# Performance work log

Hardware: AMD Instinct MI355X
Metric: run time of the kernel (lower is better)

## Reference

```python
import jax, jax.numpy as jnp
import numpy as np

B, T, D, H = 4096, 1024, 3, 64


def setup_inputs() -> dict:
    key = jax.random.key(0)
    ks = jax.random.split(key, 10)
    s_ih = 1.0 / np.sqrt(H)
    return {
        "x1": jax.random.normal(ks[0], (B, T, D), dtype=jnp.float32),
        "x2": jax.random.normal(ks[1], (B, T, D), dtype=jnp.float32),
        # PyTorch nn.GRU params, gate order (r, z, n)
        "W_ih": jax.random.uniform(ks[2], (3 * H, D), jnp.float32, -s_ih, s_ih),
        "W_hh": jax.random.uniform(ks[3], (3 * H, H), jnp.float32, -s_ih, s_ih),
        "b_ih": jax.random.uniform(ks[4], (3 * H,), jnp.float32, -s_ih, s_ih),
        "b_hh": jax.random.uniform(ks[5], (3 * H,), jnp.float32, -s_ih, s_ih),
        # MLP head: Linear(64,32) -> ReLU -> Linear(32,1) -> Sigmoid
        "W1": jax.random.uniform(ks[6], (32, H), jnp.float32, -s_ih, s_ih),
        "b1": jax.random.uniform(ks[7], (32,), jnp.float32, -s_ih, s_ih),
        "W2": jax.random.uniform(ks[8], (1, 32), jnp.float32, -1 / np.sqrt(32), 1 / np.sqrt(32)),
        "b2": jax.random.uniform(ks[9], (1,), jnp.float32, -1 / np.sqrt(32), 1 / np.sqrt(32)),
    }


def _gru_last_hidden(x, W_ih, W_hh, b_ih, b_hh):
    # x: [B, T, D] -> final hidden state [B, H], PyTorch GRU semantics.
    xs = jnp.swapaxes(x, 0, 1)  # [T, B, D]

    def step(h, xt):
        xg = xt @ W_ih.T + b_ih            # [B, 3H]
        hg = h @ W_hh.T + b_hh             # [B, 3H]
        xr, xz, xn = jnp.split(xg, 3, axis=-1)
        hr, hz, hn = jnp.split(hg, 3, axis=-1)
        r = jax.nn.sigmoid(xr + hr)
        z = jax.nn.sigmoid(xz + hz)
        n = jnp.tanh(xn + r * hn)
        h_new = (1.0 - z) * n + z * h
        return h_new, None

    h0 = jnp.zeros((x.shape[0], W_hh.shape[1]), dtype=x.dtype)
    h_last, _ = jax.lax.scan(step, h0, xs)
    return h_last


def reference(x1, x2, W_ih, W_hh, b_ih, b_hh, W1, b1, W2, b2):
    h1 = _gru_last_hidden(x1, W_ih, W_hh, b_ih, b_hh)
    h2 = _gru_last_hidden(x2, W_ih, W_hh, b_ih, b_hh)
    diff = jnp.abs(h1 - h2)                                # [B, H]
    hid = jax.nn.relu(diff @ W1.T + b1)                    # [B, 32]
    out = jax.nn.sigmoid(hid @ W2.T + b2)                  # [B, 1]
    return out
```

## Files before the change

kernel.cpp:

```cpp
#include <hip/hip_runtime.h>
#include <math.h>

#define T_ 1024
#define D_ 3
#define H_ 64

typedef _Float16 f16x8 __attribute__((ext_vector_type(8)));
typedef float f32x4 __attribute__((ext_vector_type(4)));

__device__ __forceinline__ float sigmoid_f(float x) {
    return __builtin_amdgcn_rcpf(1.0f + __expf(-x));
}

#define MFMA(A, B, C) __builtin_amdgcn_mfma_f32_16x16x32_f16((A), (B), (C), 0, 0, 0)

__global__ __launch_bounds__(256, 2) void gru_mfma5(
    const float* __restrict__ x1, const float* __restrict__ x2,
    const float* __restrict__ W_ih, const float* __restrict__ W_hh,
    const float* __restrict__ b_ih, const float* __restrict__ b_hh,
    const float* __restrict__ W1, const float* __restrict__ b1,
    const float* __restrict__ W2, const float* __restrict__ b2,
    float* __restrict__ out)
{
    const int lane = threadIdx.x & 63;
    const int w    = threadIdx.x >> 6;
    const int c    = lane & 15;
    const int q    = lane >> 4;
    const int u    = 16 * w + c;
    const int seq0 = blockIdx.x * 8;

    const float SRZ = -1.44269504f;
    const float SN  =  2.88539008f;
    const float gsc[3] = {SRZ, SRZ, SN};

    f16x8 wf[3][2];
    #pragma unroll
    for (int g = 0; g < 3; ++g)
        #pragma unroll
        for (int ks = 0; ks < 2; ++ks) {
            const float* p = W_hh + (size_t)(g * 64 + u) * H_ + 32 * ks + q * 8;
            f16x8 v;
            #pragma unroll
            for (int j = 0; j < 8; ++j) v[j] = (_Float16)(p[j] * gsc[g]);
            wf[g][ks] = v;
        }

    f16x8 bxf[3];
    #pragma unroll
    for (int g = 0; g < 3; ++g) {
        f16x8 v = {};
        if (q == 0) {
            #pragma unroll
            for (int d = 0; d < 3; ++d)
                v[d] = (_Float16)(W_ih[(size_t)(g * 64 + u) * D_ + d] * gsc[g]);
        }
        bxf[g] = v;
    }

    const float comb_r = (b_ih[u]      + b_hh[u])      * SRZ;
    const float comb_z = (b_ih[64 + u] + b_hh[64 + u]) * SRZ;
    const float bxn    = b_ih[128 + u] * SN;
    const float bhn    = b_hh[128 + u] * SN;
    const f32x4 Cr  = {comb_r, comb_r, comb_r, comb_r};
    const f32x4 Cz  = {comb_z, comb_z, comb_z, comb_z};
    const f32x4 Cxn = {bxn, bxn, bxn, bxn};
    const f32x4 Chn = {bhn, bhn, bhn, bhn};

    const float* xptr = (c < 8) ? (x1 + (size_t)(seq0 + c) * (T_ * D_))
                                : (x2 + (size_t)(seq0 + c - 8) * (T_ * D_));

    __shared__ alignas(16) _Float16 hb[2][16 * 72];
    __shared__ float dlds[8][68];

    float h[4];
    #pragma unroll
    for (int r = 0; r < 4; ++r) h[r] = 0.f;

    auto step = [&](int buf, float x0, float x1v, float x2v) {
        #pragma unroll
        for (int r = 0; r < 4; ++r)
            hb[buf][(4 * q + r) * 72 + u] = (_Float16)h[r];
        f16x8 ax = {};
        ax[0] = (_Float16)x0; ax[1] = (_Float16)x1v; ax[2] = (_Float16)x2v;
        f32x4 ar  = MFMA(ax, bxf[0], Cr);
        f32x4 az  = MFMA(ax, bxf[1], Cz);
        f32x4 axn = MFMA(ax, bxf[2], Cxn);
        __syncthreads();
        const f16x8 a0 = *(const f16x8*)&hb[buf][c * 72 + q * 8];
        const f16x8 a1 = *(const f16x8*)&hb[buf][c * 72 + 32 + q * 8];

        ar  = MFMA(a0, wf[0][0], ar);
        az  = MFMA(a0, wf[1][0], az);
        f32x4 ahn = MFMA(a0, wf[2][0], Chn);
        ar  = MFMA(a1, wf[0][1], ar);
        az  = MFMA(a1, wf[1][1], az);
        ahn = MFMA(a1, wf[2][1], ahn);

        #pragma unroll
        for (int r = 0; r < 4; ++r) {
            const float eu = __builtin_amdgcn_exp2f(ar[r]);
            const float ev = __builtin_amdgcn_exp2f(az[r]);
            const float pu = 1.0f + eu, pv = 1.0f + ev;
            const float inv = __builtin_amdgcn_rcpf(pu * pv);
            const float rr = pv * inv;
            const float zz = pu * inv;
            const float tt = axn[r] + rr * ahn[r];
            const float e2 = __builtin_amdgcn_exp2f(tt);
            const float nn = 1.0f - 2.0f * __builtin_amdgcn_rcpf(e2 + 1.0f);
            h[r] = nn + zz * (h[r] - nn);
        }
    };

    const float4* xp4 = (const float4*)xptr;
    float4 xc[3];
    #pragma unroll
    for (int i = 0; i < 3; ++i) xc[i] = xp4[i];

    for (int t = 0; t < T_; t += 4) {
        float4 xn[3];
        const int tb = (t + 4 < T_) ? (3 * (t + 4)) / 4 : (3 * t) / 4;
        #pragma unroll
        for (int i = 0; i < 3; ++i) xn[i] = xp4[tb + i];
        step(0, xc[0].x, xc[0].y, xc[0].z);
        step(1, xc[0].w, xc[1].x, xc[1].y);
        step(0, xc[1].z, xc[1].w, xc[2].x);
        step(1, xc[2].y, xc[2].z, xc[2].w);
        #pragma unroll
        for (int i = 0; i < 3; ++i) xc[i] = xn[i];
    }

    #pragma unroll
    for (int r = 0; r < 4; ++r) {
        const float o = __shfl_xor(h[r], 32);
        if (q < 2) dlds[4 * q + r][u] = fabsf(h[r] - o);
    }
    __syncthreads();
    if (w == 0) {
        const int s = lane >> 3;
        const int b = lane & 7;
        float am[4];
        #pragma unroll
        for (int i = 0; i < 4; ++i) am[i] = b1[b + 8 * i];
        #pragma unroll
        for (int k4 = 0; k4 < 16; ++k4) {
            const float4 dvec = *(const float4*)&dlds[s][k4 * 4];
            #pragma unroll
            for (int i = 0; i < 4; ++i) {
                const float4 wv = *(const float4*)&W1[(b + 8 * i) * H_ + k4 * 4];
                am[i] += dvec.x * wv.x + dvec.y * wv.y + dvec.z * wv.z + dvec.w * wv.w;
            }
        }
        float part = 0.f;
        #pragma unroll
        for (int i = 0; i < 4; ++i) part += fmaxf(am[i], 0.f) * W2[b + 8 * i];
        part += __shfl_xor(part, 1);
        part += __shfl_xor(part, 2);
        part += __shfl_xor(part, 4);
        if (b == 0) out[seq0 + s] = sigmoid_f(part + b2[0]);
    }
}

extern "C" void kernel_launch(void* const* d_in, const int* in_sizes, int n_in,
                              void* d_out, int out_size, void* d_ws, size_t ws_size,
                              hipStream_t stream) {
    const float* x1   = (const float*)d_in[0];
    const float* x2   = (const float*)d_in[1];
    const float* W_ih = (const float*)d_in[2];
    const float* W_hh = (const float*)d_in[3];
    const float* b_ih = (const float*)d_in[4];
    const float* b_hh = (const float*)d_in[5];
    const float* W1   = (const float*)d_in[6];
    const float* b1   = (const float*)d_in[7];
    const float* W2   = (const float*)d_in[8];
    const float* b2   = (const float*)d_in[9];

    const int B = in_sizes[0] / (T_ * D_);
    dim3 grid(B / 8), block(256);
    gru_mfma5<<<grid, block, 0, stream>>>(x1, x2, W_ih, W_hh, b_ih, b_hh,
                                          W1, b1, W2, b2, (float*)d_out);
}
```

Measured before the change: 578.3 us.

## Process two independent 16-sequence tiles per block to interleave MFMA chains

Each block now handles 16 batch items, running x1 and x2 sequences as two separate 16-row MFMA tiles (A and B) whose operations are interleaved within each timestep. This gives the scheduler two independent dependency chains to hide MFMA and transcendental latency, and halves the number of barriers per sequence-step. In exchange it doubles register pressure (launch bounds lowered to 1 block/CU hint), halves grid size to 256 blocks, and doubles LDS for the hidden-state buffers.

Result: slower. 718.1 us (+24.2%).

```diff
diff --git a/kernel.cpp b/kernel.cpp
--- a/kernel.cpp
+++ b/kernel.cpp
@@ -14,7 +14,7 @@
 
 #define MFMA(A, B, C) __builtin_amdgcn_mfma_f32_16x16x32_f16((A), (B), (C), 0, 0, 0)
 
-__global__ __launch_bounds__(256, 2) void gru_mfma5(
+__global__ __launch_bounds__(256, 1) void gru_mfma6(
     const float* __restrict__ x1, const float* __restrict__ x2,
     const float* __restrict__ W_ih, const float* __restrict__ W_hh,
     const float* __restrict__ b_ih, const float* __restrict__ b_hh,
@@ -27,7 +27,7 @@
     const int c    = lane & 15;
     const int q    = lane >> 4;
     const int u    = 16 * w + c;
-    const int seq0 = blockIdx.x * 8;
+    const int seq0 = blockIdx.x * 16;
 
     const float SRZ = -1.44269504f;
     const float SN  =  2.88539008f;
@@ -66,77 +66,97 @@
     const f32x4 Cxn = {bxn, bxn, bxn, bxn};
     const f32x4 Chn = {bhn, bhn, bhn, bhn};
 
-    const float* xptr = (c < 8) ? (x1 + (size_t)(seq0 + c) * (T_ * D_))
-                                : (x2 + (size_t)(seq0 + c - 8) * (T_ * D_));
-
-    __shared__ alignas(16) _Float16 hb[2][16 * 72];
-    __shared__ float dlds[8][68];
-
-    float h[4];
-    #pragma unroll
-    for (int r = 0; r < 4; ++r) h[r] = 0.f;
-
-    auto step = [&](int buf, float x0, float x1v, float x2v) {
-        #pragma unroll
-        for (int r = 0; r < 4; ++r)
-            hb[buf][(4 * q + r) * 72 + u] = (_Float16)h[r];
-        f16x8 ax = {};
-        ax[0] = (_Float16)x0; ax[1] = (_Float16)x1v; ax[2] = (_Float16)x2v;
-        f32x4 ar  = MFMA(ax, bxf[0], Cr);
-        f32x4 az  = MFMA(ax, bxf[1], Cz);
-        f32x4 axn = MFMA(ax, bxf[2], Cxn);
+    const float4* xpA = (const float4*)(x1 + (size_t)(seq0 + c) * (T_ * D_));
+    const float4* xpB = (const float4*)(x2 + (size_t)(seq0 + c) * (T_ * D_));
+
+    __shared__ alignas(16) _Float16 hb[2][2][16 * 72];
+    __shared__ float dlds[16][68];
+
+    float hA[4], hB[4];
+    #pragma unroll
+    for (int r = 0; r < 4; ++r) { hA[r] = 0.f; hB[r] = 0.f; }
+
+    auto step = [&](int buf, float a0x, float a1x, float a2x,
+                             float b0x, float b1x, float b2x) {
+        #pragma unroll
+        for (int r = 0; r < 4; ++r) {
+            hb[buf][0][(4 * q + r) * 72 + u] = (_Float16)hA[r];
+            hb[buf][1][(4 * q + r) * 72 + u] = (_Float16)hB[r];
+        }
+        f16x8 axA = {}, axB = {};
+        axA[0] = (_Float16)a0x; axA[1] = (_Float16)a1x; axA[2] = (_Float16)a2x;
+        axB[0] = (_Float16)b0x; axB[1] = (_Float16)b1x; axB[2] = (_Float16)b2x;
+        f32x4 arA  = MFMA(axA, bxf[0], Cr);
+        f32x4 arB  = MFMA(axB, bxf[0], Cr);
+        f32x4 azA  = MFMA(axA, bxf[1], Cz);
+        f32x4 azB  = MFMA(axB, bxf[1], Cz);
+        f32x4 axnA = MFMA(axA, bxf[2], Cxn);
+        f32x4 axnB = MFMA(axB, bxf[2], Cxn);
         __syncthreads();
-        const f16x8 a0 = *(const f16x8*)&hb[buf][c * 72 + q * 8];
-        const f16x8 a1 = *(const f16x8*)&hb[buf][c * 72 + 32 + q * 8];
-
-        ar  = MFMA(a0, wf[0][0], ar);
-        az  = MFMA(a0, wf[1][0], az);
-        f32x4 ahn = MFMA(a0, wf[2][0], Chn);
-        ar  = MFMA(a1, wf[0][1], ar);
-        az  = MFMA(a1, wf[1][1], az);
-        ahn = MFMA(a1, wf[2][1], ahn);
+        const f16x8 aA0 = *(const f16x8*)&hb[buf][0][c * 72 + q * 8];
+        const f16x8 aA1 = *(const f16x8*)&hb[buf][0][c * 72 + 32 + q * 8];
+        const f16x8 aB0 = *(const f16x8*)&hb[buf][1][c * 72 + q * 8];
+        const f16x8 aB1 = *(const f16x8*)&hb[buf][1][c * 72 + 32 + q * 8];
+
+        arA  = MFMA(aA0, wf[0][0], arA);
+        arB  = MFMA(aB0, wf[0][0], arB);
+        azA  = MFMA(aA0, wf[1][0], azA);
+        azB  = MFMA(aB0, wf[1][0], azB);
+        f32x4 ahnA = MFMA(aA0, wf[2][0], Chn);
+        f32x4 ahnB = MFMA(aB0, wf[2][0], Chn);
+        arA  = MFMA(aA1, wf[0][1], arA);
+        arB  = MFMA(aB1, wf[0][1], arB);
+        azA  = MFMA(aA1, wf[1][1], azA);
+        azB  = MFMA(aB1, wf[1][1], azB);
+        ahnA = MFMA(aA1, wf[2][1], ahnA);
+        ahnB = MFMA(aB1, wf[2][1], ahnB);
 
         #pragma unroll
         for (int r = 0; r < 4; ++r) {
-            const float eu = __builtin_amdgcn_exp2f(ar[r]);
-            const float ev = __builtin_amdgcn_exp2f(az[r]);
-            const float pu = 1.0f + eu, pv = 1.0f + ev;
-            const float inv = __builtin_amdgcn_rcpf(pu * pv);
-            const float rr = pv * inv;
-            const float zz = pu * inv;
-            const float tt = axn[r] + rr * ahn[r];
-            const float e2 = __builtin_amdgcn_exp2f(tt);
-            const float nn = 1.0f - 2.0f * __builtin_amdgcn_rcpf(e2 + 1.0f);
-            h[r] = nn + zz * (h[r] - nn);
+            const float euA = __builtin_amdgcn_exp2f(arA[r]);
+            const float euB = __builtin_amdgcn_exp2f(arB[r]);
+            const float evA = __builtin_amdgcn_exp2f(azA[r]);
+            const float evB = __builtin_amdgcn_exp2f(azB[r]);
+            const float puA = 1.0f + euA, pvA = 1.0f + evA;
+            const float puB = 1.0f + euB, pvB = 1.0f + evB;
+            const float invA = __builtin_amdgcn_rcpf(puA * pvA);
+            const float invB = __builtin_amdgcn_rcpf(puB * pvB);
+            const float rrA = pvA * invA, zzA = puA * invA;
+            const float rrB = pvB * invB, zzB = puB * invB;
+            const float ttA = axnA[r] + rrA * ahnA[r];
+            const float ttB = axnB[r] + rrB * ahnB[r];
+            const float e2A = __builtin_amdgcn_exp2f(ttA);
+            const float e2B = __builtin_amdgcn_exp2f(ttB);
+            const float nnA = 1.0f - 2.0f * __builtin_amdgcn_rcpf(e2A + 1.0f);
+            const float nnB = 1.0f - 2.0f * __builtin_amdgcn_rcpf(e2B + 1.0f);
+            hA[r] = nnA + zzA * (hA[r] - nnA);
+            hB[r] = nnB + zzB * (hB[r] - nnB);
         }
     };
 
-    const float4* xp4 = (const float4*)xptr;
-    float4 xc[3];
-    #pragma unroll
-    for (int i = 0; i < 3; ++i) xc[i] = xp4[i];
+    float4 xcA[3], xcB[3];
+    #pragma unroll
+    for (int i = 0; i < 3; ++i) { xcA[i] = xpA[i]; xcB[i] = xpB[i]; }
 
     for (int t = 0; t < T_; t += 4) {
-        float4 xn[3];
+        float4 xnA[3], xnB[3];
         const int tb = (t + 4 < T_) ? (3 * (t + 4)) / 4 : (3 * t) / 4;
         #pragma unroll
-        for (int i = 0; i < 3; ++i) xn[i] = xp4[tb + i];
-        step(0, xc[0].x, xc[0].y, xc[0].z);
-        step(1, xc[0].w, xc[1].x, xc[1].y);
-        step(0, xc[1].z, xc[1].w, xc[2].x);
-        step(1, xc[2].y, xc[2].z, xc[2].w);
-        #pragma unroll
-        for (int i = 0; i < 3; ++i) xc[i] = xn[i];
+        for (int i = 0; i < 3; ++i) { xnA[i] = xpA[tb + i]; xnB[i] = xpB[tb + i]; }
+        step(0, xcA[0].x, xcA[0].y, xcA[0].z, xcB[0].x, xcB[0].y, xcB[0].z);
+        step(1, xcA[0].w, xcA[1].x, xcA[1].y, xcB[0].w, xcB[1].x, xcB[1].y);
+        step(0, xcA[1].z, xcA[1].w, xcA[2].x, xcB[1].z, xcB[1].w, xcB[2].x);
+        step(1, xcA[2].y, xcA[2].z, xcA[2].w, xcB[2].y, xcB[2].z, xcB[2].w);
+        #pragma unroll
+        for (int i = 0; i < 3; ++i) { xcA[i] = xnA[i]; xcB[i] = xnB[i]; }
     }
 
     #pragma unroll
-    for (int r = 0; r < 4; ++r) {
-        const float o = __shfl_xor(h[r], 32);
-        if (q < 2) dlds[4 * q + r][u] = fabsf(h[r] - o);
-    }
+    for (int r = 0; r < 4; ++r)
+        dlds[4 * q + r][u] = fabsf(hA[r] - hB[r]);
     __syncthreads();
-    if (w == 0) {
-        const int s = lane >> 3;
+    if (w < 2) {
+        const int s = 8 * w + (lane >> 3);
         const int b = lane & 7;
         float am[4];
         #pragma unroll
@@ -175,7 +195,7 @@
     const float* b2   = (const float*)d_in[9];
 
     const int B = in_sizes[0] / (T_ * D_);
-    dim3 grid(B / 8), block(256);
-    gru_mfma5<<<grid, block, 0, stream>>>(x1, x2, W_ih, W_hh, b_ih, b_hh,
+    dim3 grid(B / 16), block(256);
+    gru_mfma6<<<grid, block, 0, stream>>>(x1, x2, W_ih, W_hh, b_ih, b_hh,
                                           W1, b1, W2, b2, (float*)d_out);
 }
```
